# Optimization experiments

Measured on AMD Instinct MI355X. Metric: run time of the kernel, lower is better.

Reference implementation:

```python
import jax, jax.numpy as jnp
import numpy as np

THRESH = 0.1        # Huber threshold (self.threshold)
CORR_WT = 1.0       # corr_wt
ENTROPY_WT = 0.0001 # entropy_wt
BS, N = 32, 1024    # n_pts = nv = 1024 hardcoded in multi_pose_with_pts


def setup_inputs() -> dict:
    key = jax.random.key(0)
    ks = jax.random.split(key, 7)
    return {
        "points_1": jax.random.normal(ks[0], (BS, N, 3), jnp.float32),
        "points_2": jax.random.normal(ks[1], (BS, N, 3), jnp.float32),
        "assign_mat_1": jax.random.normal(ks[2], (BS, N, N), jnp.float32),
        "assign_mat_2": jax.random.normal(ks[3], (BS, N, N), jnp.float32),
        "scale": jax.random.uniform(ks[4], (BS,), jnp.float32, 0.5, 1.5),
        "rotation": jax.random.normal(ks[5], (BS, 3, 3), jnp.float32),
        "translation": jax.random.normal(ks[6], (BS, 3), jnp.float32),
    }


def _transform(sRt, pts):
    # apply 4x4 pose to [b, n, 3] points (homogeneous, keep xyz)
    return jnp.einsum('bij,bnj->bni', sRt[:, :3, :3], pts) + sRt[:, :3, 3][:, None, :]


def _chamfer(x, y):
    # squared pairwise distances [b, n, m]; loss = mean min both directions
    d = (jnp.sum(x * x, -1)[:, :, None] + jnp.sum(y * y, -1)[:, None, :]
         - 2.0 * jnp.einsum('bnd,bmd->bnm', x, y))
    d = jnp.maximum(d, 0.0)
    return jnp.mean(jnp.min(d, axis=2)) + jnp.mean(jnp.min(d, axis=1))


def _corr(a, b):
    # smooth-L1-like (Huber) correspondence loss
    diff = jnp.abs(a - b)
    loss = jnp.where(diff > THRESH, diff - THRESH / 2.0, diff * diff / (2.0 * THRESH))
    return CORR_WT * jnp.mean(jnp.sum(loss, axis=2))


def _entropy(assign_mat, soft_assign, axis):
    log_assign = jax.nn.log_softmax(assign_mat, axis=axis)
    return ENTROPY_WT * jnp.mean(-jnp.sum(soft_assign * log_assign, axis=axis))


def _cos_loss(m1, m2, eps=1e-8):
    a = m1.reshape(m1.shape[0], -1)
    b = m2.reshape(m2.shape[0], -1)
    na = jnp.maximum(jnp.linalg.norm(a, axis=1), eps)
    nb = jnp.maximum(jnp.linalg.norm(b, axis=1), eps)
    return jnp.mean(1.0 - jnp.sum(a * b, axis=1) / (na * nb))


def reference(points_1, points_2, assign_mat_1, assign_mat_2, scale, rotation, translation):
    sa1 = jax.nn.softmax(assign_mat_1, axis=2)
    sa2 = jax.nn.softmax(assign_mat_2, axis=2)

    # pose_dict_RT: sRt = [[s*R, t], [0, 1]]
    sR = rotation * scale[:, None, None]
    sRt = jnp.concatenate([sR, translation[:, :, None]], axis=2)          # b 3 4
    bottom = jnp.broadcast_to(jnp.array([0., 0., 0., 1.], sRt.dtype), (sRt.shape[0], 1, 4))
    sRt12 = jnp.concatenate([sRt, bottom], axis=1)                        # b 4 4
    sRt21 = jnp.linalg.inv(sRt12)

    p1in2 = jnp.einsum('bnm,bmd->bnd', sa1, points_2)
    p2in1 = jnp.einsum('bnm,bmd->bnd', sa2, points_1)
    p1to2 = _transform(sRt12, points_1)
    p2to1 = _transform(sRt21, points_2)

    cd1 = _chamfer(p1to2, p1in2)
    cd2 = _chamfer(p2to1, p2in1)
    total = (cd1 + cd2
             + _corr(p1in2, p1to2) + _corr(p2in1, p2to1)
             + _entropy(assign_mat_1, sa1, 2) + _entropy(assign_mat_2, sa2, 2)
             + _cos_loss(assign_mat_1, assign_mat_2)
             + _entropy(assign_mat_1, sa1, 1) + _entropy(assign_mat_2, sa2, 1))
    return total
```

## Files before the change

kernel.cpp:

```cpp
#include <hip/hip_runtime.h>
#include <math.h>

#define BSZ 32
#define NP  1024

#define OFF_ACC    0
#define OFF_COS    8
#define OFF_COLC1  104
#define OFF_COLT1  (OFF_COLC1 + 32768)
#define OFF_COLC2  (OFF_COLC1 + 65536)
#define OFF_COLT2  (OFF_COLC1 + 98304)
#define ZERO_FLOATS (OFF_COLC1 + 131072)
#define OFF_MIN    ZERO_FLOATS
#define OFF_POSE   (OFF_MIN + 131072)
#define OFF_P1TO2  (OFF_POSE + 768)
#define OFF_P2TO1  (OFF_P1TO2 + 98304)
#define OFF_P1IN2  (OFF_P2TO1 + 98304)
#define OFF_P2IN1  (OFF_P1IN2 + 98304)

__global__ void k_pose(const float* __restrict__ scale,
                       const float* __restrict__ rot,
                       const float* __restrict__ tr,
                       float* __restrict__ pose) {
    int b = threadIdx.x;
    if (b >= BSZ) return;
    float s = scale[b];
    float M[9];
#pragma unroll
    for (int i = 0; i < 9; ++i) M[i] = rot[b * 9 + i] * s;
    float t0 = tr[b * 3 + 0], t1 = tr[b * 3 + 1], t2 = tr[b * 3 + 2];
    float det = M[0] * (M[4] * M[8] - M[5] * M[7])
              - M[1] * (M[3] * M[8] - M[5] * M[6])
              + M[2] * (M[3] * M[7] - M[4] * M[6]);
    float id = 1.0f / det;
    float inv[9];
    inv[0] =  (M[4] * M[8] - M[5] * M[7]) * id;
    inv[1] = -(M[1] * M[8] - M[2] * M[7]) * id;
    inv[2] =  (M[1] * M[5] - M[2] * M[4]) * id;
    inv[3] = -(M[3] * M[8] - M[5] * M[6]) * id;
    inv[4] =  (M[0] * M[8] - M[2] * M[6]) * id;
    inv[5] = -(M[0] * M[5] - M[2] * M[3]) * id;
    inv[6] =  (M[3] * M[7] - M[4] * M[6]) * id;
    inv[7] = -(M[0] * M[7] - M[1] * M[6]) * id;
    inv[8] =  (M[0] * M[4] - M[1] * M[3]) * id;
    float u0 = -(inv[0] * t0 + inv[1] * t1 + inv[2] * t2);
    float u1 = -(inv[3] * t0 + inv[4] * t1 + inv[5] * t2);
    float u2 = -(inv[6] * t0 + inv[7] * t1 + inv[8] * t2);
    float* P = pose + b * 24;
#pragma unroll
    for (int i = 0; i < 9; ++i) P[i] = M[i];
    P[9] = t0; P[10] = t1; P[11] = t2;
#pragma unroll
    for (int i = 0; i < 9; ++i) P[12 + i] = inv[i];
    P[21] = u0; P[22] = u1; P[23] = u2;
}

__global__ void k_transform(const float* __restrict__ p1, const float* __restrict__ p2,
                            const float* __restrict__ pose,
                            float* __restrict__ p1to2, float* __restrict__ p2to1) {
    int idx = blockIdx.x * 256 + threadIdx.x;
    int b = idx >> 10;
    const float* P = pose + b * 24;
    float x = p1[idx * 3 + 0], y = p1[idx * 3 + 1], z = p1[idx * 3 + 2];
    p1to2[idx * 3 + 0] = P[0] * x + P[1] * y + P[2] * z + P[9];
    p1to2[idx * 3 + 1] = P[3] * x + P[4] * y + P[5] * z + P[10];
    p1to2[idx * 3 + 2] = P[6] * x + P[7] * y + P[8] * z + P[11];
    x = p2[idx * 3 + 0]; y = p2[idx * 3 + 1]; z = p2[idx * 3 + 2];
    p2to1[idx * 3 + 0] = P[12] * x + P[13] * y + P[14] * z + P[21];
    p2to1[idx * 3 + 1] = P[15] * x + P[16] * y + P[17] * z + P[22];
    p2to1[idx * 3 + 2] = P[18] * x + P[19] * y + P[20] * z + P[23];
}

__global__ __launch_bounds__(256) void k_big(
    const float* __restrict__ am1, const float* __restrict__ am2,
    const float* __restrict__ pts1, const float* __restrict__ pts2,
    float* __restrict__ p1in2, float* __restrict__ p2in1,
    float* __restrict__ colC1, float* __restrict__ colT1,
    float* __restrict__ colC2, float* __restrict__ colT2,
    float* __restrict__ cosacc, float* __restrict__ acc) {
    const int b  = blockIdx.x >> 4;
    const int rb = blockIdx.x & 15;
    const int wv = threadIdx.x >> 6;
    const int ln = threadIdx.x & 63;
    const int row0 = rb * 64 + wv * 16;

    float pA[16][3];
    float pB[16][3];
#pragma unroll
    for (int j = 0; j < 4; ++j)
#pragma unroll
        for (int k = 0; k < 4; ++k) {
            int c = 256 * j + 4 * ln + k;
            int i = 4 * j + k;
            pA[i][0] = pts2[(b * NP + c) * 3 + 0];
            pA[i][1] = pts2[(b * NP + c) * 3 + 1];
            pA[i][2] = pts2[(b * NP + c) * 3 + 2];
            pB[i][0] = pts1[(b * NP + c) * 3 + 0];
            pB[i][1] = pts1[(b * NP + c) * 3 + 1];
            pB[i][2] = pts1[(b * NP + c) * 3 + 2];
        }

    float C1[16], T1[16], C2[16], T2[16];
#pragma unroll
    for (int i = 0; i < 16; ++i) { C1[i] = 0.f; T1[i] = 0.f; C2[i] = 0.f; T2[i] = 0.f; }
    float dacc = 0.f, n1a = 0.f, n2a = 0.f, e2a = 0.f, sSa = 0.f;

    const float4* rA = (const float4*)(am1 + ((size_t)b * NP + row0) * NP);
    const float4* rB = (const float4*)(am2 + ((size_t)b * NP + row0) * NP);

#pragma unroll 1
    for (int r = 0; r < 16; ++r) {
        float4 a[4], c4[4];
#pragma unroll
        for (int j = 0; j < 4; ++j) {
            a[j]  = rA[(size_t)r * 256 + ln + 64 * j];
            c4[j] = rB[(size_t)r * 256 + ln + 64 * j];
        }
#pragma unroll
        for (int j = 0; j < 4; ++j) {
            dacc += a[j].x * c4[j].x + a[j].y * c4[j].y + a[j].z * c4[j].z + a[j].w * c4[j].w;
            n1a  += a[j].x * a[j].x + a[j].y * a[j].y + a[j].z * a[j].z + a[j].w * a[j].w;
            n2a  += c4[j].x * c4[j].x + c4[j].y * c4[j].y + c4[j].z * c4[j].z + c4[j].w * c4[j].w;
        }
        {
            float R = 0.f, Su = 0.f, q0 = 0.f, q1 = 0.f, q2 = 0.f;
#pragma unroll
            for (int j = 0; j < 4; ++j) {
                float* e = (float*)&a[j];
#pragma unroll
                for (int k = 0; k < 4; ++k) {
                    int i = 4 * j + k;
                    float v  = e[k];
                    float ex = __expf(v);
                    R += ex; Su += ex * v;
                    q0 += ex * pA[i][0]; q1 += ex * pA[i][1]; q2 += ex * pA[i][2];
                    C1[i] += ex;
                    e[k] = ex;
                }
            }
#pragma unroll
            for (int m = 1; m < 64; m <<= 1) {
                R  += __shfl_xor(R, m);  Su += __shfl_xor(Su, m);
                q0 += __shfl_xor(q0, m); q1 += __shfl_xor(q1, m); q2 += __shfl_xor(q2, m);
            }
            float inv = 1.0f / R;
#pragma unroll
            for (int j = 0; j < 4; ++j) {
                float* e = (float*)&a[j];
#pragma unroll
                for (int k = 0; k < 4; ++k) T1[4 * j + k] += e[k] * inv;
            }
            float S = Su * inv;
            if (ln == 0) {
                e2a += __logf(R) - S;
                sSa += S;
                int row = b * NP + row0 + r;
                p1in2[row * 3 + 0] = q0 * inv;
                p1in2[row * 3 + 1] = q1 * inv;
                p1in2[row * 3 + 2] = q2 * inv;
            }
        }
        {
            float R = 0.f, Su = 0.f, q0 = 0.f, q1 = 0.f, q2 = 0.f;
#pragma unroll
            for (int j = 0; j < 4; ++j) {
                float* e = (float*)&c4[j];
#pragma unroll
                for (int k = 0; k < 4; ++k) {
                    int i = 4 * j + k;
                    float v  = e[k];
                    float ex = __expf(v);
                    R += ex; Su += ex * v;
                    q0 += ex * pB[i][0]; q1 += ex * pB[i][1]; q2 += ex * pB[i][2];
                    C2[i] += ex;
                    e[k] = ex;
                }
            }
#pragma unroll
            for (int m = 1; m < 64; m <<= 1) {
                R  += __shfl_xor(R, m);  Su += __shfl_xor(Su, m);
                q0 += __shfl_xor(q0, m); q1 += __shfl_xor(q1, m); q2 += __shfl_xor(q2, m);
            }
            float inv = 1.0f / R;
#pragma unroll
            for (int j = 0; j < 4; ++j) {
                float* e = (float*)&c4[j];
#pragma unroll
                for (int k = 0; k < 4; ++k) T2[4 * j + k] += e[k] * inv;
            }
            float S = Su * inv;
            if (ln == 0) {
                e2a += __logf(R) - S;
                sSa += S;
                int row = b * NP + row0 + r;
                p2in1[row * 3 + 0] = q0 * inv;
                p2in1[row * 3 + 1] = q1 * inv;
                p2in1[row * 3 + 2] = q2 * inv;
            }
        }
    }

#pragma unroll
    for (int j = 0; j < 4; ++j)
#pragma unroll
        for (int k = 0; k < 4; ++k) {
            int i = 4 * j + k;
            int o = b * NP + 256 * j + 4 * ln + k;
            atomicAdd(&colC1[o], C1[i]);
            atomicAdd(&colT1[o], T1[i]);
            atomicAdd(&colC2[o], C2[i]);
            atomicAdd(&colT2[o], T2[i]);
        }
#pragma unroll
    for (int m = 1; m < 64; m <<= 1) {
        dacc += __shfl_xor(dacc, m);
        n1a  += __shfl_xor(n1a, m);
        n2a  += __shfl_xor(n2a, m);
    }
    if (ln == 0) {
        atomicAdd(&cosacc[b], dacc);
        atomicAdd(&cosacc[32 + b], n1a);
        atomicAdd(&cosacc[64 + b], n2a);
        atomicAdd(&acc[0], e2a);
        atomicAdd(&acc[1], sSa);
    }
}

__global__ void k_cols(const float* __restrict__ colC1, const float* __restrict__ colT1,
                       const float* __restrict__ colC2, const float* __restrict__ colT2,
                       float* __restrict__ acc) {
    int idx = blockIdx.x * 256 + threadIdx.x;
    float v;
    if (idx < 32768) v = colT1[idx] * __logf(colC1[idx]);
    else { int i2 = idx - 32768; v = colT2[i2] * __logf(colC2[i2]); }
#pragma unroll
    for (int m = 1; m < 64; m <<= 1) v += __shfl_xor(v, m);
    if ((threadIdx.x & 63) == 0) atomicAdd(&acc[2], v);
}

__global__ __launch_bounds__(256) void k_chamfer(
    const float* __restrict__ p1to2, const float* __restrict__ p1in2,
    const float* __restrict__ p2to1, const float* __restrict__ p2in1,
    float* __restrict__ minarr) {
    int blk   = blockIdx.x;
    int chunk = blk & 3;
    int b     = (blk >> 2) & 31;
    int dir   = (blk >> 7) & 1;
    int pair  = blk >> 8;
    const float* X; const float* Y;
    if (pair == 0) { X = dir ? p1in2 : p1to2; Y = dir ? p1to2 : p1in2; }
    else           { X = dir ? p2in1 : p2to1; Y = dir ? p2to1 : p2in1; }
    __shared__ float ys[256 * 3];
    int t = threadIdx.x;
    int yi = b * NP + chunk * 256 + t;
    ys[t * 3 + 0] = Y[yi * 3 + 0];
    ys[t * 3 + 1] = Y[yi * 3 + 1];
    ys[t * 3 + 2] = Y[yi * 3 + 2];
    __syncthreads();
    float* marr = minarr + ((size_t)(pair * 2 + dir) * 32 + b) * NP;
    float x0[4], x1[4], x2[4], mn[4];
#pragma unroll
    for (int i = 0; i < 4; ++i) {
        int xi = b * NP + i * 256 + t;
        x0[i] = X[xi * 3 + 0]; x1[i] = X[xi * 3 + 1]; x2[i] = X[xi * 3 + 2];
        mn[i] = 3.0e38f;
    }
    for (int o = 0; o < 256; ++o) {
        float y0 = ys[o * 3 + 0], y1 = ys[o * 3 + 1], y2 = ys[o * 3 + 2];
#pragma unroll
        for (int i = 0; i < 4; ++i) {
            float d0 = x0[i] - y0, d1 = x1[i] - y1, d2 = x2[i] - y2;
            float d = d0 * d0 + d1 * d1 + d2 * d2;
            mn[i] = fminf(mn[i], d);
        }
    }
#pragma unroll
    for (int i = 0; i < 4; ++i)
        atomicMin((unsigned int*)&marr[i * 256 + t], __float_as_uint(mn[i]));
}

__global__ void k_corr(const float* __restrict__ p1in2, const float* __restrict__ p1to2,
                       const float* __restrict__ p2in1, const float* __restrict__ p2to1,
                       float* __restrict__ acc) {
    int idx = blockIdx.x * 256 + threadIdx.x;
    const float* A; const float* P;
    int i = idx;
    if (i < 32768) { A = p1in2; P = p1to2; }
    else           { A = p2in1; P = p2to1; i -= 32768; }
    float s = 0.f;
#pragma unroll
    for (int d = 0; d < 3; ++d) {
        float df = fabsf(A[i * 3 + d] - P[i * 3 + d]);
        s += (df > 0.1f) ? (df - 0.05f) : (df * df * 5.0f);
    }
#pragma unroll
    for (int m = 1; m < 64; m <<= 1) s += __shfl_xor(s, m);
    if ((threadIdx.x & 63) == 0) atomicAdd(&acc[3], s);
}

__global__ void k_minsum(const float* __restrict__ minarr, float* __restrict__ acc) {
    int idx = blockIdx.x * 256 + threadIdx.x;
    float v = minarr[idx];
#pragma unroll
    for (int m = 1; m < 64; m <<= 1) v += __shfl_xor(v, m);
    if ((threadIdx.x & 63) == 0) atomicAdd(&acc[4], v);
}

__global__ void k_final(const float* __restrict__ acc, const float* __restrict__ cosacc,
                        float* __restrict__ out) {
    if (threadIdx.x != 0) return;
    const float invBN = 1.0f / 32768.0f;
    float ent2 = 1e-4f * acc[0] * invBN;
    float ent1 = 1e-4f * (acc[2] - acc[1]) * invBN;
    float corr = acc[3] * invBN;
    float cham = acc[4] * invBN;
    float cosl = 0.f;
    for (int b = 0; b < 32; ++b) {
        float dot = cosacc[b];
        float na = fmaxf(sqrtf(cosacc[32 + b]), 1e-8f);
        float nb = fmaxf(sqrtf(cosacc[64 + b]), 1e-8f);
        cosl += 1.0f - dot / (na * nb);
    }
    cosl *= (1.0f / 32.0f);
    out[0] = cham + corr + ent2 + ent1 + cosl;
}

extern "C" void kernel_launch(void* const* d_in, const int* in_sizes, int n_in,
                              void* d_out, int out_size, void* d_ws, size_t ws_size,
                              hipStream_t stream) {
    const float* p1    = (const float*)d_in[0];
    const float* p2    = (const float*)d_in[1];
    const float* am1   = (const float*)d_in[2];
    const float* am2   = (const float*)d_in[3];
    const float* scale = (const float*)d_in[4];
    const float* rot   = (const float*)d_in[5];
    const float* tr    = (const float*)d_in[6];

    float* ws = (float*)d_ws;
    float* acc    = ws + OFF_ACC;
    float* cosacc = ws + OFF_COS;
    float* colC1  = ws + OFF_COLC1;
    float* colT1  = ws + OFF_COLT1;
    float* colC2  = ws + OFF_COLC2;
    float* colT2  = ws + OFF_COLT2;
    float* minarr = ws + OFF_MIN;
    float* pose   = ws + OFF_POSE;
    float* p1to2  = ws + OFF_P1TO2;
    float* p2to1  = ws + OFF_P2TO1;
    float* p1in2  = ws + OFF_P1IN2;
    float* p2in1  = ws + OFF_P2IN1;

    hipMemsetAsync(ws, 0, ZERO_FLOATS * sizeof(float), stream);
    hipMemsetAsync(minarr, 0x7F, 131072 * sizeof(float), stream);

    k_pose<<<1, 64, 0, stream>>>(scale, rot, tr, pose);
    k_transform<<<128, 256, 0, stream>>>(p1, p2, pose, p1to2, p2to1);
    k_big<<<512, 256, 0, stream>>>(am1, am2, p1, p2, p1in2, p2in1,
                                   colC1, colT1, colC2, colT2, cosacc, acc);
    k_cols<<<256, 256, 0, stream>>>(colC1, colT1, colC2, colT2, acc);
    k_chamfer<<<512, 256, 0, stream>>>(p1to2, p1in2, p2to1, p2in1, minarr);
    k_corr<<<256, 256, 0, stream>>>(p1in2, p1to2, p2in1, p2to1, acc);
    k_minsum<<<512, 256, 0, stream>>>(minarr, acc);
    k_final<<<1, 64, 0, stream>>>(acc, cosacc, (float*)d_out);
}
```

Baseline: 493.5 us.

## Fuse transform, chamfer, corr into one kernel; reduce column sums via LDS partials

Drops the memsets and the separate transform, corr, minsum and column-log kernels. The point transform moves inline into a new chamfer kernel that keeps all 1024 targets in LDS, so each thread owns a full row minimum and no atomicMin array is needed; it also computes the Huber correspondence term. The big kernel now uses 1024 blocks of 8 rows with an occupancy hint, and accumulates column partials in shared memory with LDS atomics, writing per-block partials that a separate kernel reduces before taking the log. Accumulators are zeroed inside the pose kernel. The per-block partials add global traffic, and the chamfer now uses the expanded-norm distance form.

```diff
diff --git a/kernel.cpp b/kernel.cpp
--- a/kernel.cpp
+++ b/kernel.cpp
@@ -4,26 +4,24 @@
 #define BSZ 32
 #define NP  1024
 
-#define OFF_ACC    0
-#define OFF_COS    8
-#define OFF_COLC1  104
-#define OFF_COLT1  (OFF_COLC1 + 32768)
-#define OFF_COLC2  (OFF_COLC1 + 65536)
-#define OFF_COLT2  (OFF_COLC1 + 98304)
-#define ZERO_FLOATS (OFF_COLC1 + 131072)
-#define OFF_MIN    ZERO_FLOATS
-#define OFF_POSE   (OFF_MIN + 131072)
-#define OFF_P1TO2  (OFF_POSE + 768)
-#define OFF_P2TO1  (OFF_P1TO2 + 98304)
-#define OFF_P1IN2  (OFF_P2TO1 + 98304)
-#define OFF_P2IN1  (OFF_P1IN2 + 98304)
+#define OFF_ACC   0
+#define OFF_COS   8
+#define OFF_POSE  104
+#define OFF_P1IN2 872
+#define OFF_P2IN1 (OFF_P1IN2 + 3 * BSZ * NP)
+#define OFF_COLP  (OFF_P2IN1 + 3 * BSZ * NP)
 
 __global__ void k_pose(const float* __restrict__ scale,
                        const float* __restrict__ rot,
                        const float* __restrict__ tr,
-                       float* __restrict__ pose) {
-    int b = threadIdx.x;
-    if (b >= BSZ) return;
+                       float* __restrict__ ws) {
+    int t = threadIdx.x;
+    if (t < 52) {
+        ws[OFF_ACC + 2 * t]     = 0.f;
+        ws[OFF_ACC + 2 * t + 1] = 0.f;
+    }
+    if (t >= BSZ) return;
+    int b = t;
     float s = scale[b];
     float M[9];
 #pragma unroll
@@ -46,7 +44,7 @@
     float u0 = -(inv[0] * t0 + inv[1] * t1 + inv[2] * t2);
     float u1 = -(inv[3] * t0 + inv[4] * t1 + inv[5] * t2);
     float u2 = -(inv[6] * t0 + inv[7] * t1 + inv[8] * t2);
-    float* P = pose + b * 24;
+    float* P = ws + OFF_POSE + b * 24;
 #pragma unroll
     for (int i = 0; i < 9; ++i) P[i] = M[i];
     P[9] = t0; P[10] = t1; P[11] = t2;
@@ -55,34 +53,20 @@
     P[21] = u0; P[22] = u1; P[23] = u2;
 }
 
-__global__ void k_transform(const float* __restrict__ p1, const float* __restrict__ p2,
-                            const float* __restrict__ pose,
-                            float* __restrict__ p1to2, float* __restrict__ p2to1) {
-    int idx = blockIdx.x * 256 + threadIdx.x;
-    int b = idx >> 10;
-    const float* P = pose + b * 24;
-    float x = p1[idx * 3 + 0], y = p1[idx * 3 + 1], z = p1[idx * 3 + 2];
-    p1to2[idx * 3 + 0] = P[0] * x + P[1] * y + P[2] * z + P[9];
-    p1to2[idx * 3 + 1] = P[3] * x + P[4] * y + P[5] * z + P[10];
-    p1to2[idx * 3 + 2] = P[6] * x + P[7] * y + P[8] * z + P[11];
-    x = p2[idx * 3 + 0]; y = p2[idx * 3 + 1]; z = p2[idx * 3 + 2];
-    p2to1[idx * 3 + 0] = P[12] * x + P[13] * y + P[14] * z + P[21];
-    p2to1[idx * 3 + 1] = P[15] * x + P[16] * y + P[17] * z + P[22];
-    p2to1[idx * 3 + 2] = P[18] * x + P[19] * y + P[20] * z + P[23];
-}
-
-__global__ __launch_bounds__(256) void k_big(
+__global__ __launch_bounds__(256, 3) void k_big(
     const float* __restrict__ am1, const float* __restrict__ am2,
     const float* __restrict__ pts1, const float* __restrict__ pts2,
     float* __restrict__ p1in2, float* __restrict__ p2in1,
-    float* __restrict__ colC1, float* __restrict__ colT1,
-    float* __restrict__ colC2, float* __restrict__ colT2,
-    float* __restrict__ cosacc, float* __restrict__ acc) {
-    const int b  = blockIdx.x >> 4;
-    const int rb = blockIdx.x & 15;
+    float* __restrict__ colPart, float* __restrict__ cosacc, float* __restrict__ acc) {
+    __shared__ float cacc[4096];
+    const int b  = blockIdx.x >> 5;
+    const int rb = blockIdx.x & 31;
     const int wv = threadIdx.x >> 6;
     const int ln = threadIdx.x & 63;
-    const int row0 = rb * 64 + wv * 16;
+    const int row0 = rb * 32 + wv * 8;
+
+    for (int i = threadIdx.x; i < 4096; i += 256) cacc[i] = 0.f;
+    __syncthreads();
 
     float pA[16][3];
     float pB[16][3];
@@ -109,7 +93,7 @@
     const float4* rB = (const float4*)(am2 + ((size_t)b * NP + row0) * NP);
 
 #pragma unroll 1
-    for (int r = 0; r < 16; ++r) {
+    for (int r = 0; r < 8; ++r) {
         float4 a[4], c4[4];
 #pragma unroll
         for (int j = 0; j < 4; ++j) {
@@ -205,11 +189,11 @@
 #pragma unroll
         for (int k = 0; k < 4; ++k) {
             int i = 4 * j + k;
-            int o = b * NP + 256 * j + 4 * ln + k;
-            atomicAdd(&colC1[o], C1[i]);
-            atomicAdd(&colT1[o], T1[i]);
-            atomicAdd(&colC2[o], C2[i]);
-            atomicAdd(&colT2[o], T2[i]);
+            int c = 256 * j + 4 * ln + k;
+            atomicAdd(&cacc[c],        C1[i]);
+            atomicAdd(&cacc[1024 + c], T1[i]);
+            atomicAdd(&cacc[2048 + c], C2[i]);
+            atomicAdd(&cacc[3072 + c], T2[i]);
         }
 #pragma unroll
     for (int m = 1; m < 64; m <<= 1) {
@@ -224,86 +208,101 @@
         atomicAdd(&acc[0], e2a);
         atomicAdd(&acc[1], sSa);
     }
-}
-
-__global__ void k_cols(const float* __restrict__ colC1, const float* __restrict__ colT1,
-                       const float* __restrict__ colC2, const float* __restrict__ colT2,
-                       float* __restrict__ acc) {
+    __syncthreads();
+    float4* cp = (float4*)(colPart + (size_t)blockIdx.x * 4096);
+    const float4* cs = (const float4*)cacc;
+    for (int i = threadIdx.x; i < 1024; i += 256) cp[i] = cs[i];
+}
+
+__global__ void k_colred(const float* __restrict__ colPart, float* __restrict__ acc) {
     int idx = blockIdx.x * 256 + threadIdx.x;
-    float v;
-    if (idx < 32768) v = colT1[idx] * __logf(colC1[idx]);
-    else { int i2 = idx - 32768; v = colT2[i2] * __logf(colC2[i2]); }
+    int b = idx >> 11;
+    int m = (idx >> 10) & 1;
+    int c = idx & 1023;
+    const float* p = colPart + (size_t)b * 32 * 4096 + m * 2048 + c;
+    float C = 0.f, T = 0.f;
+#pragma unroll
+    for (int rbi = 0; rbi < 32; ++rbi) {
+        C += p[rbi * 4096];
+        T += p[rbi * 4096 + 1024];
+    }
+    float v = T * __logf(C);
+#pragma unroll
+    for (int mm = 1; mm < 64; mm <<= 1) v += __shfl_xor(v, mm);
+    if ((threadIdx.x & 63) == 0) atomicAdd(&acc[2], v);
+}
+
+__global__ __launch_bounds__(256) void k_cham(
+    const float* __restrict__ p1, const float* __restrict__ p2,
+    const float* __restrict__ p1in2, const float* __restrict__ p2in1,
+    const float* __restrict__ pose, float* __restrict__ acc) {
+    __shared__ float4 ys[NP];
+    const int blk   = blockIdx.x;
+    const int chunk = blk & 3;
+    const int b     = (blk >> 2) & 31;
+    const int dir   = (blk >> 7) & 1;
+    const int pair  = blk >> 8;
+    const float* P   = pose + b * 24 + pair * 12;
+    const float* raw = pair ? p2 : p1;
+    const float* inA = pair ? p2in1 : p1in2;
+    const int t = threadIdx.x;
+
+    float m0 = P[0], m1 = P[1], m2 = P[2];
+    float m3 = P[3], m4 = P[4], m5 = P[5];
+    float m6 = P[6], m7 = P[7], m8 = P[8];
+    float t0 = P[9], t1 = P[10], t2 = P[11];
+
+#pragma unroll
+    for (int i = 0; i < 4; ++i) {
+        int q = t + 256 * i;
+        int gi = (b * NP + q) * 3;
+        float x, y, z;
+        if (dir == 0) { x = inA[gi]; y = inA[gi + 1]; z = inA[gi + 2]; }
+        else {
+            float rx = raw[gi], ry = raw[gi + 1], rz = raw[gi + 2];
+            x = m0 * rx + m1 * ry + m2 * rz + t0;
+            y = m3 * rx + m4 * ry + m5 * rz + t1;
+            z = m6 * rx + m7 * ry + m8 * rz + t2;
+        }
+        ys[q] = make_float4(x, y, z, x * x + y * y + z * z);
+    }
+    __syncthreads();
+
+    int xi = chunk * 256 + t;
+    int gx = (b * NP + xi) * 3;
+    float x0, x1, x2;
+    if (dir == 0) {
+        float rx = raw[gx], ry = raw[gx + 1], rz = raw[gx + 2];
+        x0 = m0 * rx + m1 * ry + m2 * rz + t0;
+        x1 = m3 * rx + m4 * ry + m5 * rz + t1;
+        x2 = m6 * rx + m7 * ry + m8 * rz + t2;
+    } else { x0 = inA[gx]; x1 = inA[gx + 1]; x2 = inA[gx + 2]; }
+    float sx = x0 * x0 + x1 * x1 + x2 * x2;
+
+    float mn = 3.0e38f;
+#pragma unroll 4
+    for (int o = 0; o < NP; ++o) {
+        float4 yv = ys[o];
+        float d = fmaf(-2.0f, x0 * yv.x + x1 * yv.y + x2 * yv.z, sx + yv.w);
+        mn = fminf(mn, d);
+    }
+    mn = fmaxf(mn, 0.0f);
+
+    float v = mn;
 #pragma unroll
     for (int m = 1; m < 64; m <<= 1) v += __shfl_xor(v, m);
-    if ((threadIdx.x & 63) == 0) atomicAdd(&acc[2], v);
-}
-
-__global__ __launch_bounds__(256) void k_chamfer(
-    const float* __restrict__ p1to2, const float* __restrict__ p1in2,
-    const float* __restrict__ p2to1, const float* __restrict__ p2in1,
-    float* __restrict__ minarr) {
-    int blk   = blockIdx.x;
-    int chunk = blk & 3;
-    int b     = (blk >> 2) & 31;
-    int dir   = (blk >> 7) & 1;
-    int pair  = blk >> 8;
-    const float* X; const float* Y;
-    if (pair == 0) { X = dir ? p1in2 : p1to2; Y = dir ? p1to2 : p1in2; }
-    else           { X = dir ? p2in1 : p2to1; Y = dir ? p2to1 : p2in1; }
-    __shared__ float ys[256 * 3];
-    int t = threadIdx.x;
-    int yi = b * NP + chunk * 256 + t;
-    ys[t * 3 + 0] = Y[yi * 3 + 0];
-    ys[t * 3 + 1] = Y[yi * 3 + 1];
-    ys[t * 3 + 2] = Y[yi * 3 + 2];
-    __syncthreads();
-    float* marr = minarr + ((size_t)(pair * 2 + dir) * 32 + b) * NP;
-    float x0[4], x1[4], x2[4], mn[4];
-#pragma unroll
-    for (int i = 0; i < 4; ++i) {
-        int xi = b * NP + i * 256 + t;
-        x0[i] = X[xi * 3 + 0]; x1[i] = X[xi * 3 + 1]; x2[i] = X[xi * 3 + 2];
-        mn[i] = 3.0e38f;
-    }
-    for (int o = 0; o < 256; ++o) {
-        float y0 = ys[o * 3 + 0], y1 = ys[o * 3 + 1], y2 = ys[o * 3 + 2];
-#pragma unroll
-        for (int i = 0; i < 4; ++i) {
-            float d0 = x0[i] - y0, d1 = x1[i] - y1, d2 = x2[i] - y2;
-            float d = d0 * d0 + d1 * d1 + d2 * d2;
-            mn[i] = fminf(mn[i], d);
-        }
-    }
-#pragma unroll
-    for (int i = 0; i < 4; ++i)
-        atomicMin((unsigned int*)&marr[i * 256 + t], __float_as_uint(mn[i]));
-}
-
-__global__ void k_corr(const float* __restrict__ p1in2, const float* __restrict__ p1to2,
-                       const float* __restrict__ p2in1, const float* __restrict__ p2to1,
-                       float* __restrict__ acc) {
-    int idx = blockIdx.x * 256 + threadIdx.x;
-    const float* A; const float* P;
-    int i = idx;
-    if (i < 32768) { A = p1in2; P = p1to2; }
-    else           { A = p2in1; P = p2to1; i -= 32768; }
-    float s = 0.f;
-#pragma unroll
-    for (int d = 0; d < 3; ++d) {
-        float df = fabsf(A[i * 3 + d] - P[i * 3 + d]);
-        s += (df > 0.1f) ? (df - 0.05f) : (df * df * 5.0f);
-    }
-#pragma unroll
-    for (int m = 1; m < 64; m <<= 1) s += __shfl_xor(s, m);
-    if ((threadIdx.x & 63) == 0) atomicAdd(&acc[3], s);
-}
-
-__global__ void k_minsum(const float* __restrict__ minarr, float* __restrict__ acc) {
-    int idx = blockIdx.x * 256 + threadIdx.x;
-    float v = minarr[idx];
-#pragma unroll
-    for (int m = 1; m < 64; m <<= 1) v += __shfl_xor(v, m);
-    if ((threadIdx.x & 63) == 0) atomicAdd(&acc[4], v);
+    if ((t & 63) == 0) atomicAdd(&acc[4], v);
+
+    if (dir == 0) {
+        float4 a = ys[xi];
+        float s = 0.f;
+        float d0 = fabsf(a.x - x0); s += (d0 > 0.1f) ? (d0 - 0.05f) : (d0 * d0 * 5.0f);
+        float d1 = fabsf(a.y - x1); s += (d1 > 0.1f) ? (d1 - 0.05f) : (d1 * d1 * 5.0f);
+        float d2 = fabsf(a.z - x2); s += (d2 > 0.1f) ? (d2 - 0.05f) : (d2 * d2 * 5.0f);
+#pragma unroll
+        for (int m = 1; m < 64; m <<= 1) s += __shfl_xor(s, m);
+        if ((t & 63) == 0) atomicAdd(&acc[3], s);
+    }
 }
 
 __global__ void k_final(const float* __restrict__ acc, const float* __restrict__ cosacc,
@@ -337,29 +336,17 @@
     const float* tr    = (const float*)d_in[6];
 
     float* ws = (float*)d_ws;
-    float* acc    = ws + OFF_ACC;
-    float* cosacc = ws + OFF_COS;
-    float* colC1  = ws + OFF_COLC1;
-    float* colT1  = ws + OFF_COLT1;
-    float* colC2  = ws + OFF_COLC2;
-    float* colT2  = ws + OFF_COLT2;
-    float* minarr = ws + OFF_MIN;
-    float* pose   = ws + OFF_POSE;
-    float* p1to2  = ws + OFF_P1TO2;
-    float* p2to1  = ws + OFF_P2TO1;
-    float* p1in2  = ws + OFF_P1IN2;
-    float* p2in1  = ws + OFF_P2IN1;
-
-    hipMemsetAsync(ws, 0, ZERO_FLOATS * sizeof(float), stream);
-    hipMemsetAsync(minarr, 0x7F, 131072 * sizeof(float), stream);
-
-    k_pose<<<1, 64, 0, stream>>>(scale, rot, tr, pose);
-    k_transform<<<128, 256, 0, stream>>>(p1, p2, pose, p1to2, p2to1);
-    k_big<<<512, 256, 0, stream>>>(am1, am2, p1, p2, p1in2, p2in1,
-                                   colC1, colT1, colC2, colT2, cosacc, acc);
-    k_cols<<<256, 256, 0, stream>>>(colC1, colT1, colC2, colT2, acc);
-    k_chamfer<<<512, 256, 0, stream>>>(p1to2, p1in2, p2to1, p2in1, minarr);
-    k_corr<<<256, 256, 0, stream>>>(p1in2, p1to2, p2in1, p2to1, acc);
-    k_minsum<<<512, 256, 0, stream>>>(minarr, acc);
+    float* acc     = ws + OFF_ACC;
+    float* cosacc  = ws + OFF_COS;
+    float* pose    = ws + OFF_POSE;
+    float* p1in2   = ws + OFF_P1IN2;
+    float* p2in1   = ws + OFF_P2IN1;
+    float* colPart = ws + OFF_COLP;
+
+    k_pose<<<1, 64, 0, stream>>>(scale, rot, tr, ws);
+    k_big<<<1024, 256, 0, stream>>>(am1, am2, p1, p2, p1in2, p2in1,
+                                    colPart, cosacc, acc);
+    k_colred<<<256, 256, 0, stream>>>(colPart, acc);
+    k_cham<<<512, 256, 0, stream>>>(p1, p2, p1in2, p2in1, pose, acc);
     k_final<<<1, 64, 0, stream>>>(acc, cosacc, (float*)d_out);
 }
```

After: 814.2 us. 65.0% more time.
